# Kernel tuning notes

Hardware: AMD Instinct MI355X
Metric: run time of the kernel (lower is better)

Reference implementation:

```python
import jax, jax.numpy as jnp
import numpy as np

B, H, W, C = 8, 50, 50, 256
N_ROIS = 256
ROI_SIZE = 28  # >= pool grid so every bin is non-empty


def setup_inputs() -> dict:
    key = jax.random.key(0)
    k1, k2, k3, k4 = jax.random.split(key, 4)
    feat = jax.random.normal(k1, (B, H, W, C), dtype=jnp.float32)
    batch_idx = jax.random.randint(k2, (N_ROIS,), 0, B)
    x1 = jax.random.randint(k3, (N_ROIS,), 0, W - ROI_SIZE + 1)
    y1 = jax.random.randint(k4, (N_ROIS,), 0, H - ROI_SIZE + 1)
    # rois: (image_index, x1, y1, x2, y2), inclusive coordinates
    rois = jnp.stack([batch_idx, x1, y1, x1 + ROI_SIZE - 1, y1 + ROI_SIZE - 1], axis=1).astype(jnp.int32)
    return {"feat": feat, "rois": rois, "pool_height": 7, "pool_width": 7}


def _roi_max_pool(feat, rois, ph, pw):
    n = rois.shape[0]
    h, w = feat.shape[1], feat.shape[2]
    c = feat.shape[3]
    img, x1, y1, x2, y2 = (rois[:, i] for i in range(5))
    roi_h = (y2 - y1 + 1)  # [N]
    roi_w = (x2 - x1 + 1)

    # Per-pixel bin assignment (adaptive partition): bin = floor(offset * pool / extent)
    dy = jnp.arange(h)[None, :] - y1[:, None]                      # [N,H]
    dx = jnp.arange(w)[None, :] - x1[:, None]                      # [N,W]
    row_bin = jnp.minimum(dy * ph // roi_h[:, None], ph - 1)       # [N,H]
    col_bin = jnp.minimum(dx * pw // roi_w[:, None], pw - 1)       # [N,W]
    row_ok = (dy >= 0) & (dy < roi_h[:, None])
    col_ok = (dx >= 0) & (dx < roi_w[:, None])

    valid = row_ok[:, :, None] & col_ok[:, None, :]                # [N,H,W]
    bin_id = row_bin[:, :, None] * pw + col_bin[:, None, :]        # [N,H,W]
    seg = jnp.arange(n)[:, None, None] * (ph * pw) + bin_id
    dump = n * ph * pw  # junk segment for out-of-ROI pixels
    seg = jnp.where(valid, seg, dump)

    feat_n = feat[img]                                             # [N,H,W,C] gather per ROI
    out = jax.ops.segment_max(
        feat_n.reshape(n * h * w, c), seg.reshape(n * h * w),
        num_segments=n * ph * pw + 1,
    )[: n * ph * pw]
    return out.reshape(n, ph, pw, c)                               # [N,ph,pw,C]


def reference(feat, rois, pool_height, pool_width):
    return _roi_max_pool(feat, rois, int(pool_height), int(pool_width))
```

## Files before the change

kernel.cpp:

```cpp
#include <hip/hip_runtime.h>

constexpr int Hf = 50, Wf = 50, Cf = 256;
constexpr int PH = 7, PW = 7, NB = PH * PW;
constexpr int C4 = Cf / 4;
constexpr int NXCD = 8;

typedef float f32x4 __attribute__((ext_vector_type(4)));

__global__ __launch_bounds__(256) void sort_rois_kernel(
    const int* __restrict__ rois, int n_rois, int n_images,
    int* __restrict__ hdr,
    int4* __restrict__ meta) {
  __shared__ int cnt[64], base[64];
  for (int i = threadIdx.x; i < n_images; i += blockDim.x) cnt[i] = 0;
  __syncthreads();
  for (int t = threadIdx.x; t < n_rois; t += blockDim.x)
    atomicAdd(&cnt[rois[t * 5]], 1);
  __syncthreads();
  if (threadIdx.x == 0) {
    int acc = 0;
    for (int i = 0; i < n_images; ++i) {
      base[i] = acc;
      hdr[i] = cnt[i];
      hdr[n_images + i] = acc;
      acc += cnt[i];
    }
  }
  __syncthreads();
  for (int t = threadIdx.x; t < n_rois; t += blockDim.x) {
    const int* r = rois + t * 5;
    int slot = atomicAdd(&base[r[0]], 1);
    meta[2 * slot]     = make_int4(r[0], r[1], r[2], t);
    meta[2 * slot + 1] = make_int4(r[3], r[4], 0, 0);
  }
}

__global__ __launch_bounds__(256) void pool_kernel(
    const float4* __restrict__ feat,
    const int*    __restrict__ hdr,
    const int4*   __restrict__ meta,
    float4*       __restrict__ out,
    int n_images, int bpi) {
  int j = blockIdx.x % n_images;
  int t = blockIdx.x / n_images;
  int cnt    = hdr[j];
  int sbase  = hdr[n_images + j];
  int nb_img = cnt * NB;
  int lane = threadIdx.x & 63;
  int wv   = threadIdx.x >> 6;

  for (int lb = t * 4 + wv; lb < nb_img; lb += bpi * 4) {
    int q  = lb / NB;
    int rb = lb - q * NB;
    int s  = sbase + q;

    int4 m0 = meta[2 * s];
    int4 m1 = meta[2 * s + 1];
    int img = m0.x, x1 = m0.y, y1 = m0.z, n = m0.w;
    int roi_h = m1.y - y1 + 1;
    int roi_w = m1.x - x1 + 1;

    int py = rb / PW;
    int px = rb - py * PW;

    const float4* fb = feat + (size_t)img * (Hf * Wf * C4) + lane;
    float4 m = make_float4(-INFINITY, -INFINITY, -INFINITY, -INFINITY);

    if (roi_h == 28 && roi_w == 28) {
      const float4* p0 = fb + (size_t)(y1 + 4 * py) * (Wf * C4)
                            + (size_t)(x1 + 4 * px) * C4;
#pragma unroll
      for (int dy = 0; dy < 4; ++dy) {
        const float4* prow = p0 + (size_t)dy * (Wf * C4);
#pragma unroll
        for (int dx = 0; dx < 4; ++dx) {
          float4 v = prow[(size_t)dx * C4];
          m.x = fmaxf(m.x, v.x);
          m.y = fmaxf(m.y, v.y);
          m.z = fmaxf(m.z, v.z);
          m.w = fmaxf(m.w, v.w);
        }
      }
    } else {
      int hs = (py * roi_h + PH - 1) / PH;
      int he = ((py + 1) * roi_h + PH - 1) / PH;
      int ws = (px * roi_w + PW - 1) / PW;
      int we = ((px + 1) * roi_w + PW - 1) / PW;
      for (int dy = hs; dy < he; ++dy) {
        const float4* prow = fb + (size_t)(y1 + dy) * (Wf * C4);
        for (int dx = ws; dx < we; ++dx) {
          float4 v = prow[(size_t)(x1 + dx) * C4];
          m.x = fmaxf(m.x, v.x);
          m.y = fmaxf(m.y, v.y);
          m.z = fmaxf(m.z, v.z);
          m.w = fmaxf(m.w, v.w);
        }
      }
    }

    f32x4 val = {m.x, m.y, m.z, m.w};
    __builtin_nontemporal_store(
        val, (f32x4*)(out + ((size_t)n * NB + rb) * C4 + lane));
  }
}

extern "C" void kernel_launch(void* const* d_in, const int* in_sizes, int n_in,
                              void* d_out, int out_size, void* d_ws, size_t ws_size,
                              hipStream_t stream) {
  const float* feat = (const float*)d_in[0];
  const int*   rois = (const int*)d_in[1];
  int n_rois   = in_sizes[1] / 5;
  int n_images = in_sizes[0] / (Hf * Wf * Cf);
  if (n_images < 1) n_images = 1;

  int*  hdr  = (int*)d_ws;
  int4* meta = (int4*)((char*)d_ws + 256);

  sort_rois_kernel<<<1, 256, 0, stream>>>(rois, n_rois, n_images, hdr, meta);

  int avg  = (n_rois + n_images - 1) / n_images;
  int bpi  = (2 * avg * NB + 3) / 4;
  int blocks = n_images * bpi;
  pool_kernel<<<blocks, 256, 0, stream>>>(
      (const float4*)feat, hdr, meta, (float4*)d_out, n_images, bpi);
}
```

Measured before the change: 83.70 us.

## Fuse ROI sorting into pool kernel via per-block ballot bucketing

Drops the separate single-block sort kernel. Each pool block now redundantly buckets ROIs by image using wave ballots and shared memory, then processes its image's bins. This removes one kernel launch and the dependency between the two kernels. In exchange every block repeats the small sort prologue, adds several barriers, and now reads the raw rois array instead of packed metadata. The over-subscription factor per image also drops from 2x to 1.5x, and a general fallback path is added for large inputs.

Result: slower. 87.37 us (+4.4%).

```diff
diff --git a/kernel.cpp b/kernel.cpp
--- a/kernel.cpp
+++ b/kernel.cpp
@@ -3,62 +3,74 @@
 constexpr int Hf = 50, Wf = 50, Cf = 256;
 constexpr int PH = 7, PW = 7, NB = PH * PW;
 constexpr int C4 = Cf / 4;
-constexpr int NXCD = 8;
+constexpr int MAXR = 256;
+constexpr int MAXI = 64;
 
 typedef float f32x4 __attribute__((ext_vector_type(4)));
 
-__global__ __launch_bounds__(256) void sort_rois_kernel(
-    const int* __restrict__ rois, int n_rois, int n_images,
-    int* __restrict__ hdr,
-    int4* __restrict__ meta) {
-  __shared__ int cnt[64], base[64];
-  for (int i = threadIdx.x; i < n_images; i += blockDim.x) cnt[i] = 0;
-  __syncthreads();
-  for (int t = threadIdx.x; t < n_rois; t += blockDim.x)
-    atomicAdd(&cnt[rois[t * 5]], 1);
-  __syncthreads();
-  if (threadIdx.x == 0) {
-    int acc = 0;
-    for (int i = 0; i < n_images; ++i) {
-      base[i] = acc;
-      hdr[i] = cnt[i];
-      hdr[n_images + i] = acc;
-      acc += cnt[i];
-    }
-  }
-  __syncthreads();
-  for (int t = threadIdx.x; t < n_rois; t += blockDim.x) {
-    const int* r = rois + t * 5;
-    int slot = atomicAdd(&base[r[0]], 1);
-    meta[2 * slot]     = make_int4(r[0], r[1], r[2], t);
-    meta[2 * slot + 1] = make_int4(r[3], r[4], 0, 0);
-  }
-}
-
+template <bool PINNED>
 __global__ __launch_bounds__(256) void pool_kernel(
     const float4* __restrict__ feat,
-    const int*    __restrict__ hdr,
-    const int4*   __restrict__ meta,
+    const int*    __restrict__ rois,
     float4*       __restrict__ out,
-    int n_images, int bpi) {
-  int j = blockIdx.x % n_images;
-  int t = blockIdx.x / n_images;
-  int cnt    = hdr[j];
-  int sbase  = hdr[n_images + j];
-  int nb_img = cnt * NB;
+    int n_rois, int n_images, int bpi, int n_bins) {
   int lane = threadIdx.x & 63;
   int wv   = threadIdx.x >> 6;
 
-  for (int lb = t * 4 + wv; lb < nb_img; lb += bpi * 4) {
+  __shared__ int   wcnt[4][MAXI];
+  __shared__ int   imgbase[MAXI], imgcnt[MAXI];
+  __shared__ short order[MAXR];
+
+  int basej = 0, nbloop, start, stride;
+  if (PINNED) {
+    for (int i = threadIdx.x; i < 4 * MAXI; i += 256) (&wcnt[0][0])[i] = 0;
+    __syncthreads();
+    int myimg = ((int)threadIdx.x < n_rois) ? rois[threadIdx.x * 5] : -1;
+    int rank = 0;
+    for (int im = 0; im < n_images; ++im) {
+      unsigned long long mk = __ballot(myimg == im);
+      if (myimg == im) {
+        rank = __popcll(mk & ((1ull << lane) - 1));
+        if (rank == 0) wcnt[wv][im] = __popcll(mk);
+      }
+    }
+    __syncthreads();
+    if (threadIdx.x == 0) {
+      int acc = 0;
+      for (int im = 0; im < n_images; ++im) {
+        int c = wcnt[0][im] + wcnt[1][im] + wcnt[2][im] + wcnt[3][im];
+        imgbase[im] = acc; imgcnt[im] = c; acc += c;
+      }
+    }
+    __syncthreads();
+    if (myimg >= 0) {
+      int off = imgbase[myimg] + rank;
+      for (int w = 0; w < wv; ++w) off += wcnt[w][myimg];
+      order[off] = (short)threadIdx.x;
+    }
+    __syncthreads();
+    int j  = blockIdx.x % n_images;
+    basej  = imgbase[j];
+    nbloop = imgcnt[j] * NB;
+    start  = (blockIdx.x / n_images) * 4 + wv;
+    stride = bpi * 4;
+  } else {
+    nbloop = n_bins;
+    start  = blockIdx.x * 4 + wv;
+    stride = gridDim.x * 4;
+  }
+
+  for (int lb = start; lb < nbloop; lb += stride) {
     int q  = lb / NB;
     int rb = lb - q * NB;
-    int s  = sbase + q;
+    int n  = PINNED ? (int)order[basej + q] : q;
 
-    int4 m0 = meta[2 * s];
-    int4 m1 = meta[2 * s + 1];
-    int img = m0.x, x1 = m0.y, y1 = m0.z, n = m0.w;
-    int roi_h = m1.y - y1 + 1;
-    int roi_w = m1.x - x1 + 1;
+    const int* roi = rois + n * 5;
+    int img = roi[0];
+    int x1  = roi[1];
+    int y1  = roi[2];
+    int roi_h = roi[4] - y1 + 1;
+    int roi_w = roi[3] - x1 + 1;
 
     int py = rb / PW;
     int px = rb - py * PW;
@@ -111,16 +123,18 @@
   const int*   rois = (const int*)d_in[1];
   int n_rois   = in_sizes[1] / 5;
   int n_images = in_sizes[0] / (Hf * Wf * Cf);
-  if (n_images < 1) n_images = 1;
+  int n_bins   = n_rois * NB;
+  (void)d_ws;
 
-  int*  hdr  = (int*)d_ws;
-  int4* meta = (int4*)((char*)d_ws + 256);
-
-  sort_rois_kernel<<<1, 256, 0, stream>>>(rois, n_rois, n_images, hdr, meta);
-
-  int avg  = (n_rois + n_images - 1) / n_images;
-  int bpi  = (2 * avg * NB + 3) / 4;
-  int blocks = n_images * bpi;
-  pool_kernel<<<blocks, 256, 0, stream>>>(
-      (const float4*)feat, hdr, meta, (float4*)d_out, n_images, bpi);
+  if (n_rois <= MAXR && n_images >= 1 && n_images <= MAXI) {
+    int avg = (n_rois + n_images - 1) / n_images;
+    int bpi = (avg * NB * 3 / 2 + 3) / 4;
+    pool_kernel<true><<<n_images * bpi, 256, 0, stream>>>(
+        (const float4*)feat, rois, (float4*)d_out,
+        n_rois, n_images, bpi, n_bins);
+  } else {
+    pool_kernel<false><<<(n_bins + 3) / 4, 256, 0, stream>>>(
+        (const float4*)feat, rois, (float4*)d_out,
+        n_rois, n_images, 0, n_bins);
+  }
 }
```
